# Performance work log

Measured on AMD Instinct MI355X. Metric: run time of the kernel, lower is better.

## Reference

```python
import jax, jax.numpy as jnp
import numpy as np

EMBED_DIM = 1024
NUM_HEADS = 16
HEAD_DIM = EMBED_DIM // NUM_HEADS  # 64
NUM_FEATURES = 32
POLY_DIM = 16
NUM_QUAD = 2
EPS = 1e-06
C = 2.0 + EPS
B = 4096


def setup_inputs() -> dict:
    key = jax.random.key(0)
    kx, k1, k2 = jax.random.split(key, 3)
    x = jax.random.normal(kx, (B, EMBED_DIM), dtype=jnp.float32)
    omega = jax.random.normal(k1, (NUM_QUAD, NUM_HEADS, HEAD_DIM, NUM_FEATURES), dtype=jnp.float32)
    omega = omega / jnp.sqrt(float(HEAD_DIM))
    anchors = jax.random.normal(k2, (POLY_DIM, HEAD_DIM), dtype=jnp.float32)
    anchors = anchors / jnp.linalg.norm(anchors, axis=-1, keepdims=True)
    nodes, weights = np.polynomial.laguerre.laggauss(NUM_QUAD)
    nodes = np.maximum(nodes, 0.01)
    weights = np.maximum(weights, 0.01)
    quad_nodes = jnp.array(nodes, dtype=jnp.float32) / C
    quad_weights = jnp.array(weights, dtype=jnp.float32) / C
    return {"x": x, "omega": omega, "anchors": anchors,
            "quad_nodes": quad_nodes, "quad_weights": quad_weights}


def reference(x, omega, anchors, quad_nodes, quad_weights):
    Bsz = x.shape[0]
    # [B, H, D], safe-normalize over head_dim
    xr = x.reshape(Bsz, NUM_HEADS, HEAD_DIM)
    norm = jnp.linalg.norm(xr, axis=-1, keepdims=True)
    xn = xr / jnp.maximum(norm, 1e-4)
    # polynomial features: [B, H, P]
    poly_proj = jnp.clip(jnp.einsum('bhd,pd->bhp', xn, anchors), -1.0, 1.0)
    poly_feat = poly_proj ** 2 / jnp.sqrt(float(POLY_DIM))
    # positive random features: [R, B, H, M]
    prf_proj = jnp.einsum('bhd,rhdm->rbhm', xn, omega)
    s = jnp.maximum(quad_nodes.reshape(-1, 1, 1, 1), 1e-06)
    exp_arg = jnp.clip(prf_proj * jnp.sqrt(2.0 * s) - s, -20.0, 20.0)
    prf_feat = jnp.exp(exp_arg) / jnp.sqrt(NUM_FEATURES + 1e-06)
    prf_feat = prf_feat * jnp.sqrt(jnp.maximum(quad_weights.reshape(-1, 1, 1, 1), 1e-06))
    # fused outer product over quadrature nodes: [R, B, H, P, M]
    fused = poly_feat[None, :, :, :, None] * prf_feat[:, :, :, None, :]
    # concat over r along last axis == r-major flatten: [B, R*H*P*M]
    return jnp.transpose(fused, (1, 0, 2, 3, 4)).reshape(Bsz, -1)
```

## Files before the change

kernel.cpp:

```cpp
#include <hip/hip_runtime.h>

#define NHEADS 16
#define HDIM   64
#define NFEAT  32
#define PDIM   16
#define NQUAD  2
#define GB     8
#define WAVES_PB 4

__global__ __launch_bounds__(256, 4)
void slay_kernel(const float* __restrict__ x,
                 const float* __restrict__ omega,
                 const float* __restrict__ anchors,
                 const float* __restrict__ qn,
                 const float* __restrict__ qw,
                 float* __restrict__ out)
{
    __shared__ __align__(16) float s_xn [WAVES_PB][64];
    __shared__ __align__(16) float s_prf[WAVES_PB][64];
    __shared__ __align__(16) float s_poly[WAVES_PB][16];

    const int tid  = threadIdx.x;
    const int wv   = tid >> 6;
    const int lane = tid & 63;
    const int h    = blockIdx.x & 15;
    const int b0   = ((blockIdx.x >> 4) * WAVES_PB + wv) * GB;

    const int r = lane >> 5;
    const int m = lane & 31;
    const int p = lane & 15;
    const int g = lane >> 4;

    const float sR     = fmaxf(qn[r], 1e-6f);
    const float sq2s   = sqrtf(2.0f * sR);
    const float scaleR = sqrtf(fmaxf(qw[r], 1e-6f)) / sqrtf(32.0f + 1e-6f);

    float om[64];
    {
        const float* oc = omega + ((size_t)(r * NHEADS + h) * HDIM) * NFEAT + m;
        #pragma unroll
        for (int d = 0; d < 64; ++d) om[d] = oc[(size_t)d * NFEAT];
    }
    float an[16];
    {
        const float* ac = anchors + p * HDIM + g * 16;
        #pragma unroll
        for (int dd = 0; dd < 16; ++dd) an[dd] = ac[dd];
    }

    float xvv[GB];
    {
        const float* xb = x + (size_t)b0 * (NHEADS * HDIM) + h * HDIM + lane;
        #pragma unroll
        for (int bb = 0; bb < GB; ++bb) xvv[bb] = xb[(size_t)bb * (NHEADS * HDIM)];
    }

    #pragma unroll
    for (int bb = 0; bb < GB; ++bb) {
        const int b = b0 + bb;

        float ss = xvv[bb] * xvv[bb];
        #pragma unroll
        for (int off = 32; off > 0; off >>= 1) ss += __shfl_xor(ss, off, 64);
        const float xn = xvv[bb] / fmaxf(sqrtf(ss), 1e-4f);

        __builtin_amdgcn_wave_barrier();
        s_xn[wv][lane] = xn;
        __builtin_amdgcn_wave_barrier();

        float a0 = 0.f, a1 = 0.f, a2 = 0.f, a3 = 0.f;
        #pragma unroll
        for (int d = 0; d < 64; d += 4) {
            const float s0 = __uint_as_float(__builtin_amdgcn_readlane(__float_as_uint(xn), d + 0));
            const float s1 = __uint_as_float(__builtin_amdgcn_readlane(__float_as_uint(xn), d + 1));
            const float s2 = __uint_as_float(__builtin_amdgcn_readlane(__float_as_uint(xn), d + 2));
            const float s3 = __uint_as_float(__builtin_amdgcn_readlane(__float_as_uint(xn), d + 3));
            a0 = fmaf(s0, om[d + 0], a0);
            a1 = fmaf(s1, om[d + 1], a1);
            a2 = fmaf(s2, om[d + 2], a2);
            a3 = fmaf(s3, om[d + 3], a3);
        }
        const float accR = (a0 + a1) + (a2 + a3);

        float p0 = 0.f, p1 = 0.f, p2 = 0.f, p3 = 0.f;
        #pragma unroll
        for (int q4 = 0; q4 < 4; ++q4) {
            const float4 xq = *(const float4*)&s_xn[wv][g * 16 + q4 * 4];
            p0 = fmaf(xq.x, an[q4 * 4 + 0], p0);
            p1 = fmaf(xq.y, an[q4 * 4 + 1], p1);
            p2 = fmaf(xq.z, an[q4 * 4 + 2], p2);
            p3 = fmaf(xq.w, an[q4 * 4 + 3], p3);
        }
        float accP = (p0 + p1) + (p2 + p3);
        accP += __shfl_xor(accP, 16, 64);
        accP += __shfl_xor(accP, 32, 64);

        const float arg  = fminf(fmaxf(accR * sq2s - sR, -20.f), 20.f);
        const float prf  = expf(arg) * scaleR;
        const float pc   = fminf(fmaxf(accP, -1.f), 1.f);
        const float poly = pc * pc * 0.25f;

        __builtin_amdgcn_wave_barrier();
        s_prf[wv][lane] = prf;
        if (lane < 16) s_poly[wv][lane] = poly;
        __builtin_amdgcn_wave_barrier();

        float* ob = out + (size_t)b * (NQUAD * NHEADS * PDIM * NFEAT)
                        + (size_t)h * (PDIM * NFEAT);
        #pragma unroll
        for (int i = 0; i < 4; ++i) {
            const int rr = i >> 1;
            const int pp = (i * 8 + (lane >> 3)) & 15;
            const float  pf = s_poly[wv][pp];
            const float4 pr = *(const float4*)&s_prf[wv][rr * 32 + (lane & 7) * 4];
            float4 v;
            v.x = pf * pr.x; v.y = pf * pr.y; v.z = pf * pr.z; v.w = pf * pr.w;
            *(float4*)(ob + (size_t)rr * (NHEADS * PDIM * NFEAT)
                          + (i & 1) * 256 + lane * 4) = v;
        }
    }
}

extern "C" void kernel_launch(void* const* d_in, const int* in_sizes, int n_in,
                              void* d_out, int out_size, void* d_ws, size_t ws_size,
                              hipStream_t stream)
{
    const float* x       = (const float*)d_in[0];
    const float* omega   = (const float*)d_in[1];
    const float* anchors = (const float*)d_in[2];
    const float* qn      = (const float*)d_in[3];
    const float* qw      = (const float*)d_in[4];
    float* out = (float*)d_out;

    const int Bsz = in_sizes[0] / (NHEADS * HDIM);
    dim3 grid((Bsz / (WAVES_PB * GB)) * NHEADS);
    slay_kernel<<<grid, 256, 0, stream>>>(x, omega, anchors, qn, qw, out);
}
```

Before: 62.36 us.

## Stage anchors in LDS, use nontemporal I/O, LDS broadcast for omega dot, rcp normalize

Anchors are loaded into shared memory once per block instead of into 16 registers per lane. x is now software-prefetched one row ahead with nontemporal loads instead of being loaded all up front. The omega projection reads xn from LDS as vectors instead of using readlane, and normalization uses a fast reciprocal. Output writes become nontemporal stores. Together these aim to cut register pressure, bypass cache for streaming data and reduce instruction count, at the cost of an extra block barrier and slightly less accurate division.

Measured after the change: 73.62 us. 1.18x slower.

```diff
diff --git a/kernel.cpp b/kernel.cpp
--- a/kernel.cpp
+++ b/kernel.cpp
@@ -8,6 +8,8 @@
 #define GB     8
 #define WAVES_PB 4
 
+typedef float f32x4 __attribute__((ext_vector_type(4)));
+
 __global__ __launch_bounds__(256, 4)
 void slay_kernel(const float* __restrict__ x,
                  const float* __restrict__ omega,
@@ -16,9 +18,10 @@
                  const float* __restrict__ qw,
                  float* __restrict__ out)
 {
-    __shared__ __align__(16) float s_xn [WAVES_PB][64];
-    __shared__ __align__(16) float s_prf[WAVES_PB][64];
+    __shared__ __align__(16) float s_xn  [WAVES_PB][64];
+    __shared__ __align__(16) float s_prf [WAVES_PB][64];
     __shared__ __align__(16) float s_poly[WAVES_PB][16];
+    __shared__ __align__(16) float s_anch[PDIM][68];
 
     const int tid  = threadIdx.x;
     const int wv   = tid >> 6;
@@ -31,9 +34,12 @@
     const int p = lane & 15;
     const int g = lane >> 4;
 
+    for (int i = tid; i < PDIM * HDIM; i += 256)
+        s_anch[i >> 6][i & 63] = anchors[i];
+
     const float sR     = fmaxf(qn[r], 1e-6f);
     const float sq2s   = sqrtf(2.0f * sR);
-    const float scaleR = sqrtf(fmaxf(qw[r], 1e-6f)) / sqrtf(32.0f + 1e-6f);
+    const float scaleR = sqrtf(fmaxf(qw[r], 1e-6f)) * (1.0f / sqrtf(32.0f + 1e-6f));
 
     float om[64];
     {
@@ -41,28 +47,22 @@
         #pragma unroll
         for (int d = 0; d < 64; ++d) om[d] = oc[(size_t)d * NFEAT];
     }
-    float an[16];
-    {
-        const float* ac = anchors + p * HDIM + g * 16;
-        #pragma unroll
-        for (int dd = 0; dd < 16; ++dd) an[dd] = ac[dd];
-    }
 
-    float xvv[GB];
-    {
-        const float* xb = x + (size_t)b0 * (NHEADS * HDIM) + h * HDIM + lane;
-        #pragma unroll
-        for (int bb = 0; bb < GB; ++bb) xvv[bb] = xb[(size_t)bb * (NHEADS * HDIM)];
-    }
+    __syncthreads();
 
-    #pragma unroll
+    const float* xb = x + (size_t)b0 * (NHEADS * HDIM) + h * HDIM + lane;
+    float xcur = __builtin_nontemporal_load(xb);
+
+    #pragma unroll 2
     for (int bb = 0; bb < GB; ++bb) {
-        const int b = b0 + bb;
+        float xnext = 0.0f;
+        if (bb + 1 < GB)
+            xnext = __builtin_nontemporal_load(xb + (size_t)(bb + 1) * (NHEADS * HDIM));
 
-        float ss = xvv[bb] * xvv[bb];
+        float ss = xcur * xcur;
         #pragma unroll
         for (int off = 32; off > 0; off >>= 1) ss += __shfl_xor(ss, off, 64);
-        const float xn = xvv[bb] / fmaxf(sqrtf(ss), 1e-4f);
+        const float xn = xcur * __builtin_amdgcn_rcpf(fmaxf(sqrtf(ss), 1e-4f));
 
         __builtin_amdgcn_wave_barrier();
         s_xn[wv][lane] = xn;
@@ -70,26 +70,28 @@
 
         float a0 = 0.f, a1 = 0.f, a2 = 0.f, a3 = 0.f;
         #pragma unroll
-        for (int d = 0; d < 64; d += 4) {
-            const float s0 = __uint_as_float(__builtin_amdgcn_readlane(__float_as_uint(xn), d + 0));
-            const float s1 = __uint_as_float(__builtin_amdgcn_readlane(__float_as_uint(xn), d + 1));
-            const float s2 = __uint_as_float(__builtin_amdgcn_readlane(__float_as_uint(xn), d + 2));
-            const float s3 = __uint_as_float(__builtin_amdgcn_readlane(__float_as_uint(xn), d + 3));
-            a0 = fmaf(s0, om[d + 0], a0);
-            a1 = fmaf(s1, om[d + 1], a1);
-            a2 = fmaf(s2, om[d + 2], a2);
-            a3 = fmaf(s3, om[d + 3], a3);
+        for (int d4 = 0; d4 < 16; ++d4) {
+            const f32x4 xq = *(const f32x4*)&s_xn[wv][d4 * 4];
+            a0 = fmaf(xq.x, om[d4 * 4 + 0], a0);
+            a1 = fmaf(xq.y, om[d4 * 4 + 1], a1);
+            a2 = fmaf(xq.z, om[d4 * 4 + 2], a2);
+            a3 = fmaf(xq.w, om[d4 * 4 + 3], a3);
         }
         const float accR = (a0 + a1) + (a2 + a3);
 
         float p0 = 0.f, p1 = 0.f, p2 = 0.f, p3 = 0.f;
-        #pragma unroll
-        for (int q4 = 0; q4 < 4; ++q4) {
-            const float4 xq = *(const float4*)&s_xn[wv][g * 16 + q4 * 4];
-            p0 = fmaf(xq.x, an[q4 * 4 + 0], p0);
-            p1 = fmaf(xq.y, an[q4 * 4 + 1], p1);
-            p2 = fmaf(xq.z, an[q4 * 4 + 2], p2);
-            p3 = fmaf(xq.w, an[q4 * 4 + 3], p3);
+        {
+            const float* xs = &s_xn[wv][g * 16];
+            const float* as = &s_anch[p][g * 16];
+            #pragma unroll
+            for (int q4 = 0; q4 < 4; ++q4) {
+                const f32x4 xq = *(const f32x4*)(xs + q4 * 4);
+                const f32x4 aq = *(const f32x4*)(as + q4 * 4);
+                p0 = fmaf(xq.x, aq.x, p0);
+                p1 = fmaf(xq.y, aq.y, p1);
+                p2 = fmaf(xq.z, aq.z, p2);
+                p3 = fmaf(xq.w, aq.w, p3);
+            }
         }
         float accP = (p0 + p1) + (p2 + p3);
         accP += __shfl_xor(accP, 16, 64);
@@ -105,19 +107,21 @@
         if (lane < 16) s_poly[wv][lane] = poly;
         __builtin_amdgcn_wave_barrier();
 
-        float* ob = out + (size_t)b * (NQUAD * NHEADS * PDIM * NFEAT)
+        float* ob = out + (size_t)(b0 + bb) * (NQUAD * NHEADS * PDIM * NFEAT)
                         + (size_t)h * (PDIM * NFEAT);
         #pragma unroll
         for (int i = 0; i < 4; ++i) {
             const int rr = i >> 1;
             const int pp = (i * 8 + (lane >> 3)) & 15;
-            const float  pf = s_poly[wv][pp];
-            const float4 pr = *(const float4*)&s_prf[wv][rr * 32 + (lane & 7) * 4];
-            float4 v;
+            const float pf = s_poly[wv][pp];
+            const f32x4 pr = *(const f32x4*)&s_prf[wv][rr * 32 + (lane & 7) * 4];
+            f32x4 v;
             v.x = pf * pr.x; v.y = pf * pr.y; v.z = pf * pr.z; v.w = pf * pr.w;
-            *(float4*)(ob + (size_t)rr * (NHEADS * PDIM * NFEAT)
-                          + (i & 1) * 256 + lane * 4) = v;
+            __builtin_nontemporal_store(v,
+                (f32x4*)(ob + (size_t)rr * (NHEADS * PDIM * NFEAT)
+                            + (i & 1) * 256 + lane * 4));
         }
+        xcur = xnext;
     }
 }
 
```
